# Kernel optimization log

Hardware: AMD Instinct MI355X
Metric: run time of the kernel (lower is better)

## Reference

```python
import jax, jax.numpy as jnp
import numpy as np

B, S, E, H = 4, 2048, 1024, 16
DH = E // H
EXP = 1024  # FeedForwardPart default expansion_dim
EPS = 1e-5


def layer_norm(x, gamma, beta):
    mu = jnp.mean(x, axis=-1, keepdims=True)
    var = jnp.var(x, axis=-1, keepdims=True)
    return (x - mu) * jax.lax.rsqrt(var + EPS) * gamma + beta


def setup_inputs() -> dict:
    key = jax.random.key(0)
    ks = jax.random.split(key, 8)
    s = 0.02
    return {
        "x": jax.random.normal(ks[0], (B, S, E), jnp.float32),
        "mask": jnp.ones((B, 1, 1, S), jnp.int32),
        "wq": jax.random.normal(ks[1], (E, E), jnp.float32) * s,
        "wk": jax.random.normal(ks[2], (E, E), jnp.float32) * s,
        "wv": jax.random.normal(ks[3], (E, E), jnp.float32) * s,
        "wo": jax.random.normal(ks[4], (E, E), jnp.float32) * s,
        "bo": jnp.zeros((E,), jnp.float32),
        "w1": jax.random.normal(ks[5], (E, EXP), jnp.float32) * s,
        "b1": jnp.zeros((EXP,), jnp.float32),
        "w2": jax.random.normal(ks[6], (EXP, E), jnp.float32) * s,
        "b2": jnp.zeros((E,), jnp.float32),
        "gamma": jnp.ones((E,), jnp.float32),
        "beta": jnp.zeros((E,), jnp.float32),
    }


def reference(x, mask, wq, wk, wv, wo, bo, w1, b1, w2, b2, gamma, beta):
    # Multi-head self-attention
    q = (x @ wq).reshape(B, S, H, DH)
    k = (x @ wk).reshape(B, S, H, DH)
    v = (x @ wv).reshape(B, S, H, DH)
    scores = jnp.einsum("bqhd,bkhd->bhqk", q, k) / jnp.sqrt(jnp.float32(DH))
    scores = jnp.where(mask == 0, jnp.float32(-1e10), scores)
    attn = jax.nn.softmax(scores, axis=-1)
    ctx = jnp.einsum("bhqk,bkhd->bqhd", attn, v).reshape(B, S, E)
    attn_out = ctx @ wo + bo
    # Residual + shared LayerNorm
    h = layer_norm(attn_out + x, gamma, beta)
    # FFN (expansion 1024 per source default)
    ff = jax.nn.relu(h @ w1 + b1) @ w2 + b2
    return layer_norm(ff + h, gamma, beta)
```

## Files before the change

kernel.cpp:

```cpp
#include <hip/hip_runtime.h>
#include <hip/hip_bf16.h>

typedef short s16x8 __attribute__((ext_vector_type(8)));
typedef float f32x4 __attribute__((ext_vector_type(4)));
typedef float f32x16 __attribute__((ext_vector_type(16)));
typedef unsigned short u16;

#define B_ 4
#define S_ 2048
#define E_ 1024
#define H_ 16
#define DH_ 64

__device__ __forceinline__ u16 f2b(float f) {
  union { float f; unsigned u; } x; x.f = f;
  unsigned r = (x.u + 0x7fffu + ((x.u >> 16) & 1u)) >> 16;
  return (u16)r;
}

__device__ __forceinline__ float b2f(u16 v) {
  union { unsigned u; float f; } x; x.u = ((unsigned)v) << 16; return x.f;
}

__device__ __forceinline__ unsigned pk2(float lo, float hi) {
  __hip_bfloat162 h = __float22bfloat162_rn(float2{lo, hi});
  union { __hip_bfloat162 h; unsigned u; } c; c.h = h; return c.u;
}

__device__ __forceinline__ float fexp2(float x) { return __builtin_amdgcn_exp2f(x); }

__device__ __forceinline__ void pl32swap(unsigned& x, unsigned& y) {
  asm("v_permlane32_swap_b32 %0, %1" : "+v"(x), "+v"(y));
}

__device__ __forceinline__ void async16(const void* g, void* l) {
  __builtin_amdgcn_global_load_lds((const __attribute__((address_space(1))) void*)g,
                                   (__attribute__((address_space(3))) void*)l,
                                   16, 0, 0);
}

__global__ __launch_bounds__(256) void k_cast(const float* __restrict__ in,
                                              u16* __restrict__ out, int n4) {
  int i = blockIdx.x * 256 + threadIdx.x;
  if (i >= n4) return;
  float4 v = ((const float4*)in)[i];
  ushort4 o;
  o.x = f2b(v.x); o.y = f2b(v.y); o.z = f2b(v.z); o.w = f2b(v.w);
  ((ushort4*)out)[i] = o;
}

__global__ __launch_bounds__(256) void k_castT6(
    const float* __restrict__ w0, const float* __restrict__ w1,
    const float* __restrict__ w2, const float* __restrict__ w3,
    const float* __restrict__ w4, const float* __restrict__ w5,
    u16* __restrict__ wtBase) {
  __shared__ float tile[32][33];
  const int z = blockIdx.z;
  const float* in = z == 0 ? w0 : z == 1 ? w1 : z == 2 ? w2 : z == 3 ? w3 : z == 4 ? w4 : w5;
  u16* out = wtBase + (size_t)z * (1024 * 1024);
  int k0 = blockIdx.x * 32, n0 = blockIdx.y * 32;
  int tx = threadIdx.x, ty = threadIdx.y;
#pragma unroll
  for (int i = 0; i < 32; i += 8)
    tile[ty + i][tx] = in[(long)(k0 + ty + i) * 1024 + n0 + tx];
  __syncthreads();
#pragma unroll
  for (int i = 0; i < 32; i += 8)
    out[(long)(n0 + ty + i) * 1024 + k0 + tx] = f2b(tile[tx][ty + i]);
}

__global__ __launch_bounds__(256, 2) void k_gemm(
    const u16* __restrict__ A, const u16* __restrict__ Bt,
    int N, int K,
    const float* __restrict__ bias, int relu, int mode,
    const u16* __restrict__ resB,
    float* __restrict__ outF, u16* __restrict__ outB,
    u16* __restrict__ oq, u16* __restrict__ ok, u16* __restrict__ ov) {
  __shared__ __align__(16) u16 Al[128 * 32];
  __shared__ __align__(16) u16 Bl[128 * 32];
  const int t = threadIdx.x;
  const int lane = t & 63, w = t >> 6;
  const int g = lane >> 4, li = lane & 15;
  const int wr = w >> 1, wc = w & 1;
  const int bm = blockIdx.x * 128, bn = blockIdx.y * 128;

  f32x4 acc[4][4] = {};

  const long ar0 = bm + (t >> 2), ar1 = bm + ((256 + t) >> 2);
  const long br0 = bn + (t >> 2), br1 = bn + ((256 + t) >> 2);
  const int c0 = (t & 3) * 8, c1 = ((256 + t) & 3) * 8;
  u16* aD0 = &Al[(w * 64) * 8];
  u16* aD1 = &Al[(256 + w * 64) * 8];
  u16* bD0 = &Bl[(w * 64) * 8];
  u16* bD1 = &Bl[(256 + w * 64) * 8];

  for (int kt = 0; kt < K; kt += 32) {
    async16(&A[ar0 * K + kt + c0], aD0);
    async16(&A[ar1 * K + kt + c1], aD1);
    async16(&Bt[br0 * K + kt + c0], bD0);
    async16(&Bt[br1 * K + kt + c1], bD1);
    __syncthreads();
    s16x8 af[4], bf[4];
#pragma unroll
    for (int mi = 0; mi < 4; ++mi)
      af[mi] = *(const s16x8*)&Al[(wr * 64 + mi * 16 + li) * 32 + g * 8];
#pragma unroll
    for (int nf = 0; nf < 4; ++nf)
      bf[nf] = *(const s16x8*)&Bl[(wc * 64 + nf * 16 + li) * 32 + g * 8];
#pragma unroll
    for (int mi = 0; mi < 4; ++mi)
#pragma unroll
      for (int nf = 0; nf < 4; ++nf)
        acc[mi][nf] = __builtin_amdgcn_mfma_f32_16x16x32_bf16(af[mi], bf[nf], acc[mi][nf], 0, 0, 0);
    __syncthreads();
  }

#pragma unroll
  for (int mi = 0; mi < 4; ++mi)
#pragma unroll
    for (int nf = 0; nf < 4; ++nf) {
      int col = bn + wc * 64 + nf * 16 + li;
      if (mode == 1) {
        int which = col >> 10, cc = col & 1023;
        int hh = cc >> 6, dd = cc & 63;
        u16* dst = which == 0 ? oq : (which == 1 ? ok : ov);
        float scl = which == 0 ? 0.18033688011112042f : 1.f;
#pragma unroll
        for (int r = 0; r < 4; ++r) {
          long row = bm + wr * 64 + mi * 16 + g * 4 + r;
          int b2 = (int)(row >> 11), ss = (int)(row & 2047);
          dst[(((long)b2 * H_ + hh) * S_ + ss) * DH_ + dd] = f2b(acc[mi][nf][r] * scl);
        }
      } else {
        float bv = bias ? bias[col] : 0.f;
#pragma unroll
        for (int r = 0; r < 4; ++r) {
          long row = bm + wr * 64 + mi * 16 + g * 4 + r;
          float v = acc[mi][nf][r] + bv;
          if (resB) v += b2f(resB[row * N + col]);
          if (relu) v = fmaxf(v, 0.f);
          if (outF) outF[row * N + col] = v;
          if (outB) outB[row * N + col] = f2b(v);
        }
      }
    }
}

__global__ __launch_bounds__(512) void k_attn(
    const u16* __restrict__ Q, const u16* __restrict__ Kg, const u16* __restrict__ Vg,
    const int* __restrict__ mask, u16* __restrict__ ctx) {
  __shared__ __align__(16) u16 Kl[3][64 * 64];
  __shared__ __align__(16) u16 Vt[3][64 * 72];
  __shared__ __align__(16) float MBs[S_];
  __shared__ int MFlag[S_ / 64];
  __shared__ __align__(16) float BC[8 * 32];
  const int t = threadIdx.x;
  const int lane = t & 63, wid = t >> 6;
  const int q = lane & 31, hi = lane >> 5;
  const int bh = blockIdx.x;
  const int b = bh >> 4, h = bh & 15;
  const long bhoff = (long)bh * S_ * DH_;
  const int q0 = blockIdx.y * 256 + wid * 32;
  const int skey = t >> 3, sdj = t & 7;
  const int NT = S_ / 64;

  {
    int4 m4 = ((const int4*)(mask + (long)b * S_))[t];
    float4 f;
    f.x = m4.x ? 0.f : -1e10f; f.y = m4.y ? 0.f : -1e10f;
    f.z = m4.z ? 0.f : -1e10f; f.w = m4.w ? 0.f : -1e10f;
    ((float4*)MBs)[t] = f;
    bool ok = m4.x && m4.y && m4.z && m4.w;
    unsigned long long vote = __ballot(ok);
    if ((lane & 15) == 0)
      MFlag[t >> 4] = (((vote >> ((lane >> 4) * 16)) & 0xFFFFull) == 0xFFFFull);
  }

  s16x8 qf[4];
  {
    const u16* Qp = Q + bhoff + (long)(q0 + q) * DH_;
#pragma unroll
    for (int c = 0; c < 4; ++c) qf[c] = *(const s16x8*)(Qp + c * 16 + hi * 8);
  }

  s16x8 kreg, vreg;
#define LOADKV(TI) { \
    kreg = *(const s16x8*)(Kg + bhoff + (long)((TI) * 64 + skey) * DH_ + sdj * 8); \
    vreg = *(const s16x8*)(Vg + bhoff + (long)((TI) * 64 + lane) * DH_ + wid * 8); }
#define WRITEKV(BUF) { \
    *(s16x8*)((char*)&Kl[BUF][0] + skey * 128 + ((sdj * 16) ^ ((skey & 7) << 4))) = kreg; \
    _Pragma("unroll") \
    for (int j = 0; j < 8; ++j) Vt[BUF][(wid * 8 + j) * 72 + lane] = (u16)vreg[j]; }

  const int swz = (q & 7) << 4;
#define QKSTEP(S0, S1, BUF) { \
    const char* Kc = (const char*)&Kl[BUF][0]; \
    _Pragma("unroll") \
    for (int c = 0; c < 4; ++c) { \
      s16x8 kf0 = *(const s16x8*)(Kc + q * 128 + ((c * 32 + hi * 16) ^ swz)); \
      s16x8 kf1 = *(const s16x8*)(Kc + (32 + q) * 128 + ((c * 32 + hi * 16) ^ swz)); \
      S0 = __builtin_amdgcn_mfma_f32_32x32x16_bf16(kf0, qf[c], S0, 0, 0, 0); \
      S1 = __builtin_amdgcn_mfma_f32_32x32x16_bf16(kf1, qf[c], S1, 0, 0, 0); \
    } }

#define SOFTPV(S0, S1, TI) { \
    const int kt = (TI) * 64; \
    const u16* Vc = &Vt[(TI) % 3][0]; \
    const bool mok = MFlag[TI] != 0; \
    float p[32]; \
    float t00 = -1e30f, t01 = -1e30f, t10 = -1e30f, t11 = -1e30f; \
    if (mok) { \
      _Pragma("unroll") \
      for (int j = 0; j < 16; j += 2) { \
        p[j] = S0[j]; p[j + 1] = S0[j + 1]; \
        p[16 + j] = S1[j]; p[16 + j + 1] = S1[j + 1]; \
        t00 = fmaxf(t00, S0[j]); t01 = fmaxf(t01, S0[j + 1]); \
        t10 = fmaxf(t10, S1[j]); t11 = fmaxf(t11, S1[j + 1]); \
      } \
    } else { \
      _Pragma("unroll") \
      for (int g4 = 0; g4 < 4; ++g4) { \
        f32x4 mb0 = *(const f32x4*)&MBs[kt + g4 * 8 + hi * 4]; \
        f32x4 mb1 = *(const f32x4*)&MBs[kt + 32 + g4 * 8 + hi * 4]; \
        _Pragma("unroll") \
        for (int e = 0; e < 4; ++e) { \
          float v0 = S0[g4 * 4 + e] + mb0[e]; \
          float v1 = S1[g4 * 4 + e] + mb1[e]; \
          p[g4 * 4 + e] = v0; p[16 + g4 * 4 + e] = v1; \
          if (e & 1) { t01 = fmaxf(t01, v0); t11 = fmaxf(t11, v1); } \
          else       { t00 = fmaxf(t00, v0); t10 = fmaxf(t10, v1); } \
        } \
      } \
    } \
    float tmax = fmaxf(fmaxf(t00, t01), fmaxf(t10, t11)); \
    tmax = fmaxf(tmax, __shfl_xor(tmax, 32)); \
    if (!__all(tmax <= m_run + 11.5f)) { \
      float mnew = fmaxf(m_run, tmax); \
      float corr = fexp2(m_run - mnew); \
      m_run = mnew; l_run *= corr; \
      if (lane < 32) BC[wid * 32 + q] = corr; \
      asm volatile("s_waitcnt lgkmcnt(0)" ::: "memory"); \
      _Pragma("unroll") \
      for (int g4 = 0; g4 < 4; ++g4) { \
        f32x4 cv = *(const f32x4*)&BC[wid * 32 + g4 * 8 + hi * 4]; \
        _Pragma("unroll") \
        for (int e = 0; e < 4; ++e) { o0[g4 * 4 + e] *= cv[e]; o1[g4 * 4 + e] *= cv[e]; } \
      } \
    } \
    float ps0 = 0.f, ps1 = 0.f, ps2 = 0.f, ps3 = 0.f; \
    _Pragma("unroll") \
    for (int j = 0; j < 32; j += 4) { \
      float a = fexp2(p[j] - m_run), b2v = fexp2(p[j + 1] - m_run); \
      float c = fexp2(p[j + 2] - m_run), d = fexp2(p[j + 3] - m_run); \
      p[j] = a; p[j + 1] = b2v; p[j + 2] = c; p[j + 3] = d; \
      ps0 += a; ps1 += b2v; ps2 += c; ps3 += d; \
    } \
    l_run += (ps0 + ps1) + (ps2 + ps3); \
    _Pragma("unroll") \
    for (int c = 0; c < 4; ++c) { \
      unsigned X1 = pk2(p[c * 8 + 0], p[c * 8 + 1]); \
      unsigned X2 = pk2(p[c * 8 + 2], p[c * 8 + 3]); \
      unsigned Y1 = pk2(p[c * 8 + 4], p[c * 8 + 5]); \
      unsigned Y2 = pk2(p[c * 8 + 6], p[c * 8 + 7]); \
      pl32swap(X1, Y1); pl32swap(X2, Y2); \
      union { unsigned u[4]; s16x8 v; } pu; \
      pu.u[0] = X1; pu.u[1] = X2; pu.u[2] = Y1; pu.u[3] = Y2; \
      s16x8 vb0 = *(const s16x8*)(Vc + (long)q * 72 + c * 16 + hi * 8); \
      s16x8 vb1 = *(const s16x8*)(Vc + (long)(32 + q) * 72 + c * 16 + hi * 8); \
      o0 = __builtin_amdgcn_mfma_f32_32x32x16_bf16(pu.v, vb0, o0, 0, 0, 0); \
      o1 = __builtin_amdgcn_mfma_f32_32x32x16_bf16(pu.v, vb1, o1, 0, 0, 0); \
    } }

#define ITER(I, SC0, SC1, SN0, SN1) { \
    const int ip1 = (I) + 1; \
    if (ip1 < NT) WRITEKV(ip1 % 3); \
    __syncthreads(); \
    if (ip1 < NT) { \
      SN0 = zz; SN1 = zz; \
      QKSTEP(SN0, SN1, ip1 % 3); \
      if (ip1 + 1 < NT) LOADKV(ip1 + 1); \
    } \
    SOFTPV(SC0, SC1, I); }

  f32x16 zz = {};
  f32x16 o0 = zz, o1 = zz;
  float m_run = -1e30f, l_run = 0.f;

  LOADKV(0);
  WRITEKV(0);
  __syncthreads();
  f32x16 sA0 = zz, sA1 = zz, sB0 = zz, sB1 = zz;
  QKSTEP(sA0, sA1, 0);
  LOADKV(1);

  for (int i = 0; i < NT; i += 2) {
    ITER(i, sA0, sA1, sB0, sB1);
    ITER(i + 1, sB0, sB1, sA0, sA1);
  }

  l_run += __shfl_xor(l_run, 32);
  float inv = 1.f / fmaxf(l_run, 1e-30f);
  if (lane < 32) BC[wid * 32 + q] = inv;
  asm volatile("s_waitcnt lgkmcnt(0)" ::: "memory");
#pragma unroll
  for (int g4 = 0; g4 < 4; ++g4) {
    f32x4 iv = *(const f32x4*)&BC[wid * 32 + g4 * 8 + hi * 4];
#pragma unroll
    for (int e = 0; e < 4; ++e) {
      int qr = e + g4 * 8 + hi * 4;
      long ro = ((long)(b * S_ + q0 + qr) * H_ + h) * DH_ + q;
      ctx[ro] = f2b(o0[g4 * 4 + e] * iv[e]);
      ctx[ro + 32] = f2b(o1[g4 * 4 + e] * iv[e]);
    }
  }
#undef LOADKV
#undef WRITEKV
#undef QKSTEP
#undef SOFTPV
#undef ITER
}

__global__ __launch_bounds__(256) void k_lnb(const u16* __restrict__ a, const u16* __restrict__ res,
                                             const float* __restrict__ gamma, const float* __restrict__ beta,
                                             float* __restrict__ outF, u16* __restrict__ outB) {
  const int row = blockIdx.x, t = threadIdx.x;
  const long base = (long)row * E_;
  ushort4 av = ((const ushort4*)(a + base))[t];
  float4 s = make_float4(b2f(av.x), b2f(av.y), b2f(av.z), b2f(av.w));
  if (res) {
    ushort4 rv = ((const ushort4*)(res + base))[t];
    s.x += b2f(rv.x); s.y += b2f(rv.y); s.z += b2f(rv.z); s.w += b2f(rv.w);
  }
  float ps = s.x + s.y + s.z + s.w;
  float pq = s.x * s.x + s.y * s.y + s.z * s.z + s.w * s.w;
#pragma unroll
  for (int xm = 32; xm >= 1; xm >>= 1) { ps += __shfl_xor(ps, xm); pq += __shfl_xor(pq, xm); }
  __shared__ float red[8];
  int w = t >> 6, lane = t & 63;
  if (lane == 0) { red[w] = ps; red[4 + w] = pq; }
  __syncthreads();
  ps = red[0] + red[1] + red[2] + red[3];
  pq = red[4] + red[5] + red[6] + red[7];
  float mu = ps * (1.f / E_);
  float rs = rsqrtf(pq * (1.f / E_) - mu * mu + 1e-5f);
  float4 gv = ((const float4*)gamma)[t];
  float4 be = ((const float4*)beta)[t];
  float4 o = make_float4((s.x - mu) * rs * gv.x + be.x, (s.y - mu) * rs * gv.y + be.y,
                         (s.z - mu) * rs * gv.z + be.z, (s.w - mu) * rs * gv.w + be.w);
  if (outF) ((float4*)(outF + base))[t] = o;
  if (outB) {
    ushort4 ob; ob.x = f2b(o.x); ob.y = f2b(o.y); ob.z = f2b(o.z); ob.w = f2b(o.w);
    ((ushort4*)(outB + base))[t] = ob;
  }
}

extern "C" void kernel_launch(void* const* d_in, const int* in_sizes, int n_in,
                              void* d_out, int out_size, void* d_ws, size_t ws_size,
                              hipStream_t stream) {
  const float* x  = (const float*)d_in[0];
  const int* mask = (const int*)d_in[1];
  const float* wq = (const float*)d_in[2];
  const float* wk = (const float*)d_in[3];
  const float* wv = (const float*)d_in[4];
  const float* wo = (const float*)d_in[5];
  const float* bo = (const float*)d_in[6];
  const float* w1 = (const float*)d_in[7];
  const float* b1 = (const float*)d_in[8];
  const float* w2 = (const float*)d_in[9];
  const float* b2 = (const float*)d_in[10];
  const float* gamma = (const float*)d_in[11];
  const float* beta  = (const float*)d_in[12];
  float* out = (float*)d_out;

  char* ws = (char*)d_ws;
  const size_t MB = 1024ull * 1024ull;
  u16* xb  = (u16*)(ws + 0);
  u16* wqt = (u16*)(ws + 16 * MB);
  u16* wot = (u16*)(ws + 22 * MB);
  u16* w1t = (u16*)(ws + 24 * MB);
  u16* w2t = (u16*)(ws + 26 * MB);
  u16* qb  = (u16*)(ws + 28 * MB);
  u16* kb  = (u16*)(ws + 44 * MB);
  u16* vb  = (u16*)(ws + 60 * MB);
  u16* ctx = (u16*)(ws + 76 * MB);
  u16* aob = (u16*)(ws + 92 * MB);
  u16* hb  = (u16*)(ws + 108 * MB);
  u16* ff1 = qb;
  u16* ff2b = kb;

  const int n4 = B_ * S_ * E_ / 4;
  k_cast<<<n4 / 256, 256, 0, stream>>>(x, xb, n4);
  k_castT6<<<dim3(32, 32, 6), dim3(32, 8), 0, stream>>>(wq, wk, wv, wo, w1, w2, wqt);

  k_gemm<<<dim3(64, 24), 256, 0, stream>>>(xb, wqt, 3072, 1024, nullptr, 0, 1,
                                           nullptr, nullptr, nullptr, qb, kb, vb);

  k_attn<<<dim3(B_ * H_, S_ / 256), 512, 0, stream>>>(qb, kb, vb, mask, ctx);

  dim3 gg(64, 8);
  k_gemm<<<gg, 256, 0, stream>>>(ctx, wot, 1024, 1024, bo, 0, 0, xb, nullptr, aob,
                                 nullptr, nullptr, nullptr);
  k_lnb<<<B_ * S_, 256, 0, stream>>>(aob, nullptr, gamma, beta, nullptr, hb);
  k_gemm<<<gg, 256, 0, stream>>>(hb, w1t, 1024, 1024, b1, 1, 0, nullptr, nullptr, ff1,
                                 nullptr, nullptr, nullptr);
  k_gemm<<<gg, 256, 0, stream>>>(ff1, w2t, 1024, 1024, b2, 0, 0, hb, nullptr, ff2b,
                                 nullptr, nullptr, nullptr);
  k_lnb<<<B_ * S_, 256, 0, stream>>>(ff2b, nullptr, gamma, beta, out, nullptr);
}
```

Measured before the change: 324.9 us.

## Move residual add into layernorm and streamline attention softmax max reduction

Removes the bf16 residual-add read from the GEMM epilogue and passes the residual tensor to the layernorm kernel, which presumably already accepts a second input to add. In attention, the mask bias is added in place to the score registers, the separate copy into p[] is dropped, and the cross-half max reduction uses a permlane32 swap instead of a shuffle. The aim is a lighter GEMM epilogue, fewer register moves, and a cheaper reduction in the attention inner loop. The rounding order of the residual add changes slightly, because aob is rounded to bf16 before the add.

```diff
diff --git a/kernel.cpp b/kernel.cpp
--- a/kernel.cpp
+++ b/kernel.cpp
@@ -31,6 +31,13 @@
 
 __device__ __forceinline__ void pl32swap(unsigned& x, unsigned& y) {
   asm("v_permlane32_swap_b32 %0, %1" : "+v"(x), "+v"(y));
+}
+
+__device__ __forceinline__ float pmax32(float v) {
+  union { float f; unsigned u; } a, b;
+  a.f = v; b.f = v;
+  pl32swap(a.u, b.u);
+  return fmaxf(a.f, b.f);
 }
 
 __device__ __forceinline__ void async16(const void* g, void* l) {
@@ -73,7 +80,6 @@
     const u16* __restrict__ A, const u16* __restrict__ Bt,
     int N, int K,
     const float* __restrict__ bias, int relu, int mode,
-    const u16* __restrict__ resB,
     float* __restrict__ outF, u16* __restrict__ outB,
     u16* __restrict__ oq, u16* __restrict__ ok, u16* __restrict__ ov) {
   __shared__ __align__(16) u16 Al[128 * 32];
@@ -137,7 +143,6 @@
         for (int r = 0; r < 4; ++r) {
           long row = bm + wr * 64 + mi * 16 + g * 4 + r;
           float v = acc[mi][nf][r] + bv;
-          if (resB) v += b2f(resB[row * N + col]);
           if (relu) v = fmaxf(v, 0.f);
           if (outF) outF[row * N + col] = v;
           if (outB) outB[row * N + col] = f2b(v);
@@ -206,34 +211,24 @@
 #define SOFTPV(S0, S1, TI) { \
     const int kt = (TI) * 64; \
     const u16* Vc = &Vt[(TI) % 3][0]; \
-    const bool mok = MFlag[TI] != 0; \
-    float p[32]; \
-    float t00 = -1e30f, t01 = -1e30f, t10 = -1e30f, t11 = -1e30f; \
-    if (mok) { \
-      _Pragma("unroll") \
-      for (int j = 0; j < 16; j += 2) { \
-        p[j] = S0[j]; p[j + 1] = S0[j + 1]; \
-        p[16 + j] = S1[j]; p[16 + j + 1] = S1[j + 1]; \
-        t00 = fmaxf(t00, S0[j]); t01 = fmaxf(t01, S0[j + 1]); \
-        t10 = fmaxf(t10, S1[j]); t11 = fmaxf(t11, S1[j + 1]); \
-      } \
-    } else { \
+    if (MFlag[TI] == 0) {   \
       _Pragma("unroll") \
       for (int g4 = 0; g4 < 4; ++g4) { \
         f32x4 mb0 = *(const f32x4*)&MBs[kt + g4 * 8 + hi * 4]; \
         f32x4 mb1 = *(const f32x4*)&MBs[kt + 32 + g4 * 8 + hi * 4]; \
         _Pragma("unroll") \
         for (int e = 0; e < 4; ++e) { \
-          float v0 = S0[g4 * 4 + e] + mb0[e]; \
-          float v1 = S1[g4 * 4 + e] + mb1[e]; \
-          p[g4 * 4 + e] = v0; p[16 + g4 * 4 + e] = v1; \
-          if (e & 1) { t01 = fmaxf(t01, v0); t11 = fmaxf(t11, v1); } \
-          else       { t00 = fmaxf(t00, v0); t10 = fmaxf(t10, v1); } \
+          S0[g4 * 4 + e] += mb0[e]; S1[g4 * 4 + e] += mb1[e]; \
         } \
       } \
     } \
-    float tmax = fmaxf(fmaxf(t00, t01), fmaxf(t10, t11)); \
-    tmax = fmaxf(tmax, __shfl_xor(tmax, 32)); \
+    float t00 = -1e30f, t01 = -1e30f, t10 = -1e30f, t11 = -1e30f; \
+    _Pragma("unroll") \
+    for (int j = 0; j < 16; j += 2) { \
+      t00 = fmaxf(t00, S0[j]); t01 = fmaxf(t01, S0[j + 1]); \
+      t10 = fmaxf(t10, S1[j]); t11 = fmaxf(t11, S1[j + 1]); \
+    } \
+    float tmax = pmax32(fmaxf(fmaxf(t00, t01), fmaxf(t10, t11))); \
     if (!__all(tmax <= m_run + 11.5f)) { \
       float mnew = fmaxf(m_run, tmax); \
       float corr = fexp2(m_run - mnew); \
@@ -247,13 +242,21 @@
         for (int e = 0; e < 4; ++e) { o0[g4 * 4 + e] *= cv[e]; o1[g4 * 4 + e] *= cv[e]; } \
       } \
     } \
+    float p[32]; \
     float ps0 = 0.f, ps1 = 0.f, ps2 = 0.f, ps3 = 0.f; \
     _Pragma("unroll") \
-    for (int j = 0; j < 32; j += 4) { \
-      float a = fexp2(p[j] - m_run), b2v = fexp2(p[j + 1] - m_run); \
-      float c = fexp2(p[j + 2] - m_run), d = fexp2(p[j + 3] - m_run); \
-      p[j] = a; p[j + 1] = b2v; p[j + 2] = c; p[j + 3] = d; \
-      ps0 += a; ps1 += b2v; ps2 += c; ps3 += d; \
+    for (int j = 0; j < 16; j += 4) { \
+      float a = fexp2(S0[j] - m_run), bb = fexp2(S0[j + 1] - m_run); \
+      float c = fexp2(S0[j + 2] - m_run), d = fexp2(S0[j + 3] - m_run); \
+      p[j] = a; p[j + 1] = bb; p[j + 2] = c; p[j + 3] = d; \
+      ps0 += a; ps1 += bb; ps2 += c; ps3 += d; \
+    } \
+    _Pragma("unroll") \
+    for (int j = 0; j < 16; j += 4) { \
+      float a = fexp2(S1[j] - m_run), bb = fexp2(S1[j + 1] - m_run); \
+      float c = fexp2(S1[j + 2] - m_run), d = fexp2(S1[j + 3] - m_run); \
+      p[16 + j] = a; p[16 + j + 1] = bb; p[16 + j + 2] = c; p[16 + j + 3] = d; \
+      ps0 += a; ps1 += bb; ps2 += c; ps3 += d; \
     } \
     l_run += (ps0 + ps1) + (ps2 + ps3); \
     _Pragma("unroll") \
@@ -393,17 +396,17 @@
   k_castT6<<<dim3(32, 32, 6), dim3(32, 8), 0, stream>>>(wq, wk, wv, wo, w1, w2, wqt);
 
   k_gemm<<<dim3(64, 24), 256, 0, stream>>>(xb, wqt, 3072, 1024, nullptr, 0, 1,
-                                           nullptr, nullptr, nullptr, qb, kb, vb);
+                                           nullptr, nullptr, qb, kb, vb);
 
   k_attn<<<dim3(B_ * H_, S_ / 256), 512, 0, stream>>>(qb, kb, vb, mask, ctx);
 
   dim3 gg(64, 8);
-  k_gemm<<<gg, 256, 0, stream>>>(ctx, wot, 1024, 1024, bo, 0, 0, xb, nullptr, aob,
+  k_gemm<<<gg, 256, 0, stream>>>(ctx, wot, 1024, 1024, bo, 0, 0, nullptr, aob,
                                  nullptr, nullptr, nullptr);
-  k_lnb<<<B_ * S_, 256, 0, stream>>>(aob, nullptr, gamma, beta, nullptr, hb);
-  k_gemm<<<gg, 256, 0, stream>>>(hb, w1t, 1024, 1024, b1, 1, 0, nullptr, nullptr, ff1,
+  k_lnb<<<B_ * S_, 256, 0, stream>>>(aob, xb, gamma, beta, nullptr, hb);
+  k_gemm<<<gg, 256, 0, stream>>>(hb, w1t, 1024, 1024, b1, 1, 0, nullptr, ff1,
                                  nullptr, nullptr, nullptr);
-  k_gemm<<<gg, 256, 0, stream>>>(ff1, w2t, 1024, 1024, b2, 0, 0, hb, nullptr, ff2b,
+  k_gemm<<<gg, 256, 0, stream>>>(ff1, w2t, 1024, 1024, b2, 0, 0, nullptr, ff2b,
                                  nullptr, nullptr, nullptr);
-  k_lnb<<<B_ * S_, 256, 0, stream>>>(ff2b, nullptr, gamma, beta, out, nullptr);
-}
+  k_lnb<<<B_ * S_, 256, 0, stream>>>(ff2b, hb, gamma, beta, out, nullptr);
+}
```

New measurement: 301.0 us. 7.4% less time.
